# Kernel optimization log

Measured on AMD Instinct MI355X. Metric: run time of the kernel, lower is better.

Reference implementation:

```python
import jax, jax.numpy as jnp
import numpy as np

N = {'QENT': 20000, 'CENT': 50000, 'SPAN': 40000, 'SENT': 40000}
E = 250000
IN_DIM, HID = 256, 128
NEG_SLOPE = 0.2  # GATConv default negative_slope
RELS = [('QENT', 'SPAN'), ('QENT', 'SENT'), ('CENT', 'SENT'), ('SPAN', 'CENT'), ('CENT', 'CENT')]
ENAMES = ['e_qent_span', 'e_qent_sent', 'e_cent_sent', 'e_span_cent', 'e_cent_cooccur']


def setup_inputs() -> dict:
    key = jax.random.key(0)
    ks = jax.random.split(key, 20)
    inp = {}
    for i, t in enumerate(['QENT', 'CENT', 'SPAN', 'SENT']):
        inp['x_' + t] = jax.random.normal(ks[i], (N[t], IN_DIM), jnp.float32)
    for i, (nm, (s, d)) in enumerate(zip(ENAMES, RELS)):
        k1, k2 = jax.random.split(ks[4 + i])
        src = jax.random.randint(k1, (E,), 0, N[s])
        dst = jax.random.randint(k2, (E,), 0, N[d])
        inp[nm] = jnp.stack([src, dst]).astype(jnp.int32)
    inp['lin_W'] = jax.random.normal(ks[10], (4, IN_DIM, HID), jnp.float32) / np.sqrt(IN_DIM).astype(np.float32)
    inp['lin_b'] = jnp.zeros((4, HID), jnp.float32)
    inp['conv_Ws'] = jax.random.normal(ks[11], (2, 5, HID, HID), jnp.float32) / np.sqrt(HID).astype(np.float32)
    inp['conv_Wd'] = jax.random.normal(ks[12], (2, 5, HID, HID), jnp.float32) / np.sqrt(HID).astype(np.float32)
    inp['conv_as'] = jax.random.normal(ks[13], (2, 5, HID), jnp.float32) / np.sqrt(HID).astype(np.float32)
    inp['conv_ad'] = jax.random.normal(ks[14], (2, 5, HID), jnp.float32) / np.sqrt(HID).astype(np.float32)
    inp['conv_b'] = jnp.zeros((2, 5, HID), jnp.float32)
    inp['out_W'] = jax.random.normal(ks[15], (HID, 1), jnp.float32) / np.sqrt(HID).astype(np.float32)
    inp['out_b'] = jnp.zeros((1,), jnp.float32)
    return inp


def _gat(x_src, x_dst, edge, Ws, Wd, a_s, a_d, b, n_dst):
    """PyG GATConv, heads=1, concat=True, add_self_loops=False, bipartite lin_src/lin_dst."""
    hs = x_src @ Ws                       # [Ns, H]
    hd = x_dst @ Wd                       # [Nd, H]
    src, dst = edge[0], edge[1]
    e = jax.nn.leaky_relu((hs @ a_s)[src] + (hd @ a_d)[dst], NEG_SLOPE)  # [E]
    m = jax.ops.segment_max(e, dst, num_segments=n_dst)
    m = jnp.where(jnp.isfinite(m), m, 0.0)
    ex = jnp.exp(e - m[dst])
    denom = jax.ops.segment_sum(ex, dst, num_segments=n_dst)
    alpha = ex / (denom[dst] + 1e-16)     # segment softmax (PyG adds 1e-16)
    out = jax.ops.segment_sum(alpha[:, None] * hs[src], dst, num_segments=n_dst)
    return out + b


def _forward(x_QENT, x_CENT, x_SPAN, x_SENT,
             e_qent_span, e_qent_sent, e_cent_sent, e_span_cent, e_cent_cooccur,
             lin_W, lin_b, conv_Ws, conv_Wd, conv_as, conv_ad, conv_b, out_W, out_b):
    # per-type input projection (pyg Linear has bias)
    x = {'QENT': x_QENT @ lin_W[0] + lin_b[0],
         'CENT': x_CENT @ lin_W[1] + lin_b[1],
         'SPAN': x_SPAN @ lin_W[2] + lin_b[2],
         'SENT': x_SENT @ lin_W[3] + lin_b[3]}
    for l in range(2):
        p = lambda r: (conv_Ws[l, r], conv_Wd[l, r], conv_as[l, r], conv_ad[l, r], conv_b[l, r])
        span = _gat(x['QENT'], x['SPAN'], e_qent_span, *p(0), N['SPAN'])
        sent = (_gat(x['QENT'], x['SENT'], e_qent_sent, *p(1), N['SENT'])
                + _gat(x['CENT'], x['SENT'], e_cent_sent, *p(2), N['SENT']))  # HeteroConv aggr='sum'
        cent = (_gat(x['SPAN'], x['CENT'], e_span_cent, *p(3), N['CENT'])
                + _gat(x['CENT'], x['CENT'], e_cent_cooccur, *p(4), N['CENT']))
        x = {'QENT': x['QENT'],  # QENT has no incoming edges; carried through so layer 2 can use it as source
             'SPAN': jax.nn.relu(span),
             'SENT': jax.nn.relu(sent),
             'CENT': jax.nn.relu(cent)}
    return (x['SPAN'] @ out_W + out_b)[:, 0]  # squeeze(-1) -> [N_SPAN]


def reference(x_QENT, x_CENT, x_SPAN, x_SENT,
              e_qent_span, e_qent_sent, e_cent_sent, e_span_cent, e_cent_cooccur,
              lin_W, lin_b, conv_Ws, conv_Wd, conv_as, conv_ad, conv_b, out_W, out_b):
    return _forward(x_QENT, x_CENT, x_SPAN, x_SENT,
                    e_qent_span, e_qent_sent, e_cent_sent, e_span_cent, e_cent_cooccur,
                    lin_W, lin_b, conv_Ws, conv_Wd, conv_as, conv_ad, conv_b, out_W, out_b)
```

## Files before the change

kernel.cpp:

```cpp
#include <hip/hip_runtime.h>
#include <hip/hip_fp16.h>

#define IN_DIM 256
#define HID 128
#define ELLW 16
#define OVF_CAP 32768

using bf16x8 = __attribute__((ext_vector_type(8))) short;
using f32x4 = __attribute__((ext_vector_type(4))) float;

struct h8 { __half2 a, b, c, d; };

__device__ __forceinline__ unsigned short f2bf(float f) {
    unsigned u = __float_as_uint(f);
    u += 0x7fffu + ((u >> 16) & 1u);
    return (unsigned short)(u >> 16);
}

template <int CTRL>
__device__ __forceinline__ float dpp_rot(float x) {
    return __int_as_float(
        __builtin_amdgcn_update_dpp(0, __float_as_int(x), CTRL, 0xf, 0xf, false));
}
__device__ __forceinline__ float rsum16(float x) {
    x += dpp_rot<0x121>(x);
    x += dpp_rot<0x122>(x);
    x += dpp_rot<0x124>(x);
    x += dpp_rot<0x128>(x);
    return x;
}
__device__ __forceinline__ float rmax16(float x) {
    x = fmaxf(x, dpp_rot<0x121>(x));
    x = fmaxf(x, dpp_rot<0x122>(x));
    x = fmaxf(x, dpp_rot<0x124>(x));
    x = fmaxf(x, dpp_rot<0x128>(x));
    return x;
}

__device__ __forceinline__ void accum8(f32x4& a0, f32x4& a1, float a, const h8& hv) {
    const float2 f0 = __half22float2(hv.a);
    const float2 f1 = __half22float2(hv.b);
    const float2 f2 = __half22float2(hv.c);
    const float2 f3 = __half22float2(hv.d);
    a0[0] += a * f0.x; a0[1] += a * f0.y;
    a0[2] += a * f1.x; a0[3] += a * f1.y;
    a1[0] += a * f2.x; a1[1] += a * f2.y;
    a1[2] += a * f3.x; a1[3] += a * f3.y;
}

__device__ __forceinline__ float epilogue16(const f32x4& a0, const f32x4& a1,
                                            const float* __restrict__ bias,
                                            const float* __restrict__ dvec, int sl) {
    const f32x4 bb0 = *reinterpret_cast<const f32x4*>(bias + sl * 8);
    const f32x4 bb1 = *reinterpret_cast<const f32x4*>(bias + sl * 8 + 4);
    const f32x4 d0 = *reinterpret_cast<const f32x4*>(dvec + sl * 8);
    const f32x4 d1 = *reinterpret_cast<const f32x4*>(dvec + sl * 8 + 4);
    float q = 0.f;
#pragma unroll
    for (int i = 0; i < 4; ++i) {
        q += fmaxf(a0[i] + bb0[i], 0.f) * d0[i];
        q += fmaxf(a1[i] + bb1[i], 0.f) * d1[i];
    }
    return rsum16(q);
}

__device__ __forceinline__ void wt_cvt_one(const float* __restrict__ W,
                                           short* __restrict__ Wt, int idx) {
    const int kkblk = idx >> 10;
    const int n = (idx >> 3) & 127;
    const int t = idx & 7;
    const int k = (kkblk << 3) | t;
    Wt[idx] = (short)f2bf(W[(size_t)k * HID + n]);
}

__global__ __launch_bounds__(256) void setup_k(const float* __restrict__ lin_W,
                                               const float* __restrict__ lin_b,
                                               const float* __restrict__ conv_Ws,
                                               const float* __restrict__ Wd,
                                               const float* __restrict__ adv,
                                               short* __restrict__ wtl,
                                               short* __restrict__ wtc0,
                                               short* __restrict__ wtc5,
                                               float* __restrict__ wd_out,
                                               float* __restrict__ v2,
                                               float* __restrict__ c2,
                                               int* __restrict__ deg,
                                               int* __restrict__ ell,
                                               int* __restrict__ ovf_cnt, int NS, int zd) {
    const int b = blockIdx.x;
    if (b < 256) {
        const int idx = b * 256 + threadIdx.x;
        if (idx < 32768) {
            wt_cvt_one(lin_W, wtl, idx);
        } else if (idx < 49152) {
            wt_cvt_one(conv_Ws, wtc0, idx - 32768);
        } else {
            wt_cvt_one(conv_Ws + 5 * (size_t)HID * HID, wtc5, idx - 49152);
        }
    } else if (b == 256) {
        __shared__ float wd1s[HID];
        const int t = threadIdx.x;
        const int l = t >> 7, j = t & 127;
        const float* w = Wd + ((size_t)(l * 5) * HID + j) * HID;
        const float* a = adv + (size_t)(l * 5) * HID;
        float s = 0.f;
        for (int k = 0; k < HID; k += 4) {
            const float4 wv = *reinterpret_cast<const float4*>(w + k);
            const float4 av = *reinterpret_cast<const float4*>(a + k);
            s += wv.x * av.x + wv.y * av.y + wv.z * av.z + wv.w * av.w;
        }
        wd_out[t] = s;
        if (l == 0) wd1s[j] = s;
        __syncthreads();
        const float* wr = lin_W + 2 * (size_t)IN_DIM * HID + (size_t)t * HID;
        float p = 0.f;
        for (int k = 0; k < HID; k += 4) {
            const float4 wv = *reinterpret_cast<const float4*>(wr + k);
            p += wv.x * wd1s[k] + wv.y * wd1s[k + 1] + wv.z * wd1s[k + 2] +
                 wv.w * wd1s[k + 3];
        }
        v2[t] = p;
        if (t == 0) {
            const float* br = lin_b + 2 * HID;
            float q = 0.f;
            for (int k = 0; k < HID; ++k) q += br[k] * wd1s[k];
            c2[0] = q;
        }
        if (t == 1) ovf_cnt[0] = 0;
    } else if (b < 257 + zd) {
        const int i4 = ((b - 257) * 256 + threadIdx.x) * 4;
        if (i4 + 4 <= NS) {
            *reinterpret_cast<int4*>(deg + i4) = make_int4(0, 0, 0, 0);
        } else {
            for (int i = i4; i < NS; ++i) deg[i] = 0;
        }
    } else {
        const int total = NS * ELLW;
        const int i4 = ((b - 257 - zd) * 256 + threadIdx.x) * 4;
        if (i4 + 4 <= total) *reinterpret_cast<int4*>(ell + i4) = make_int4(0, 0, 0, 0);
    }
}

template <int K>
__device__ __forceinline__ void gemm_body(const float* __restrict__ A,
                                          const short* __restrict__ Wt,
                                          const float* __restrict__ bias,
                                          float* __restrict__ C, int N, int bid) {
    const int tid = threadIdx.x;
    const int w = tid >> 6;
    const int lane = tid & 63;
    const int m16 = lane & 15;
    const int kg = lane >> 4;

    const int arow = bid * 64 + w * 16 + m16;
    const bool ok = arow < N;

    f32x4 acc[8];
#pragma unroll
    for (int j = 0; j < 8; ++j) acc[j] = (f32x4){0.f, 0.f, 0.f, 0.f};

    for (int k0 = 0; k0 < K; k0 += 32) {
        bf16x8 af = {0, 0, 0, 0, 0, 0, 0, 0};
        if (ok) {
            const float* ap = A + (size_t)arow * K + k0 + kg * 8;
            const float4 f0 = *reinterpret_cast<const float4*>(ap);
            const float4 f1 = *reinterpret_cast<const float4*>(ap + 4);
            af[0] = (short)f2bf(f0.x); af[1] = (short)f2bf(f0.y);
            af[2] = (short)f2bf(f0.z); af[3] = (short)f2bf(f0.w);
            af[4] = (short)f2bf(f1.x); af[5] = (short)f2bf(f1.y);
            af[6] = (short)f2bf(f1.z); af[7] = (short)f2bf(f1.w);
        }
        const short* bbase = Wt + (((k0 >> 3) + kg) << 10);
#pragma unroll
        for (int j = 0; j < 8; ++j) {
            const bf16x8 bf = *reinterpret_cast<const bf16x8*>(bbase + ((j * 16 + m16) << 3));
            acc[j] = __builtin_amdgcn_mfma_f32_16x16x32_bf16(af, bf, acc[j], 0, 0, 0);
        }
    }

    const int rbase = bid * 64 + w * 16 + kg * 4;
    float bj[8];
#pragma unroll
    for (int j = 0; j < 8; ++j) bj[j] = bias ? bias[j * 16 + m16] : 0.f;
#pragma unroll
    for (int j = 0; j < 8; ++j)
#pragma unroll
        for (int r = 0; r < 4; ++r) {
            const int row = rbase + r;
            if (row < N) C[(size_t)row * HID + j * 16 + m16] = acc[j][r] + bj[j];
        }
}

__global__ __launch_bounds__(256) void build_gemm_k(const int* __restrict__ src,
                                                    const int* __restrict__ dst, int E,
                                                    int* __restrict__ deg,
                                                    int* __restrict__ ell,
                                                    int2* __restrict__ ovf,
                                                    int* __restrict__ ovf_cnt,
                                                    const float* __restrict__ A,
                                                    const short* __restrict__ Wt,
                                                    const float* __restrict__ bias,
                                                    float* __restrict__ C, int N, int eb) {
    if ((int)blockIdx.x < eb) {
        const int e = blockIdx.x * 256 + threadIdx.x;
        if (e < E) {
            const int d = dst[e], s = src[e];
            const int pos = atomicAdd(deg + d, 1);
            if (pos < ELLW) {
                ell[(size_t)d * ELLW + pos] = s;
            } else {
                const int oi = atomicAdd(ovf_cnt, 1);
                if (oi < OVF_CAP) ovf[oi] = make_int2(d, s);
            }
        }
    } else {
        gemm_body<IN_DIM>(A, Wt, bias, C, N, (int)blockIdx.x - eb);
    }
}

__global__ __launch_bounds__(256) void gemm_dual_k(const float* __restrict__ A,
                                                   const short* __restrict__ Wt0,
                                                   const short* __restrict__ Wt1,
                                                   __half* __restrict__ C,
                                                   float* __restrict__ as1,
                                                   float* __restrict__ as2,
                                                   const float* __restrict__ a1v,
                                                   const float* __restrict__ a2v, int N) {
    const int tid = threadIdx.x;
    const int w = tid >> 6;
    const int lane = tid & 63;
    const int m16 = lane & 15;
    const int kg = lane >> 4;

    const int arow = blockIdx.x * 64 + w * 16 + m16;
    const bool ok = arow < N;

    f32x4 acc[16];
#pragma unroll
    for (int j = 0; j < 16; ++j) acc[j] = (f32x4){0.f, 0.f, 0.f, 0.f};

    for (int k0 = 0; k0 < HID; k0 += 32) {
        bf16x8 af = {0, 0, 0, 0, 0, 0, 0, 0};
        if (ok) {
            const float* ap = A + (size_t)arow * HID + k0 + kg * 8;
            const float4 f0 = *reinterpret_cast<const float4*>(ap);
            const float4 f1 = *reinterpret_cast<const float4*>(ap + 4);
            af[0] = (short)f2bf(f0.x); af[1] = (short)f2bf(f0.y);
            af[2] = (short)f2bf(f0.z); af[3] = (short)f2bf(f0.w);
            af[4] = (short)f2bf(f1.x); af[5] = (short)f2bf(f1.y);
            af[6] = (short)f2bf(f1.z); af[7] = (short)f2bf(f1.w);
        }
        const int boff = ((k0 >> 3) + kg) << 10;
        const short* b0 = Wt0 + boff;
        const short* b1 = Wt1 + boff;
#pragma unroll
        for (int j = 0; j < 8; ++j) {
            const bf16x8 bf0 = *reinterpret_cast<const bf16x8*>(b0 + ((j * 16 + m16) << 3));
            acc[j] = __builtin_amdgcn_mfma_f32_16x16x32_bf16(af, bf0, acc[j], 0, 0, 0);
            const bf16x8 bf1 = *reinterpret_cast<const bf16x8*>(b1 + ((j * 16 + m16) << 3));
            acc[j + 8] = __builtin_amdgcn_mfma_f32_16x16x32_bf16(af, bf1, acc[j + 8], 0, 0, 0);
        }
    }

    const int rbase = blockIdx.x * 64 + w * 16 + kg * 4;
#pragma unroll
    for (int j = 0; j < 16; ++j)
#pragma unroll
        for (int r = 0; r < 4; ++r) {
            const int row = rbase + r;
            if (row < N) C[(size_t)row * 256 + j * 16 + m16] = __float2half(acc[j][r]);
        }

    float p1[4] = {0.f, 0.f, 0.f, 0.f};
    float p2[4] = {0.f, 0.f, 0.f, 0.f};
#pragma unroll
    for (int j = 0; j < 8; ++j) {
        const float a1 = a1v[j * 16 + m16];
        const float a2 = a2v[j * 16 + m16];
#pragma unroll
        for (int r = 0; r < 4; ++r) {
            p1[r] += acc[j][r] * a1;
            p2[r] += acc[j + 8][r] * a2;
        }
    }
#pragma unroll
    for (int r = 0; r < 4; ++r) {
        p1[r] = rsum16(p1[r]);
        p2[r] = rsum16(p2[r]);
    }
    if (m16 == 0)
#pragma unroll
        for (int r = 0; r < 4; ++r) {
            const int row = rbase + r;
            if (row < N) {
                as1[row] = p1[r];
                as2[row] = p2[r];
            }
        }
}

__global__ __launch_bounds__(256, 4) void gat_fused_k(
    const int* __restrict__ deg_arr, const int* __restrict__ ell,
    const int2* __restrict__ ovf, const int* __restrict__ ovf_cnt_p,
    const float* __restrict__ x_span, const float* __restrict__ v2,
    const float* __restrict__ c2, const float* __restrict__ as1,
    const float* __restrict__ as2, const __half* __restrict__ hs,
    const float* __restrict__ b1, const float* __restrict__ wd2v,
    const float* __restrict__ b2, const float* __restrict__ outW,
    const float* __restrict__ outb, float* __restrict__ out, int Ndst) {
    const int gidx = blockIdx.x * blockDim.x + threadIdx.x;
    const int row = gidx >> 4;
    const int sl = threadIdx.x & 15;
    const int grp = threadIdx.x & 48;
    if (row >= Ndst) return;

    const int deg = deg_arr[row];
    const int ce = ell[(size_t)row * ELLW + sl];

    float p = 0.f;
    const float* xr = x_span + (size_t)row * IN_DIM + sl * 16;
    const float* vr = v2 + sl * 16;
#pragma unroll
    for (int i = 0; i < 4; ++i) {
        const float4 xv = *reinterpret_cast<const float4*>(xr + i * 4);
        const float4 vv = *reinterpret_cast<const float4*>(vr + i * 4);
        p += xv.x * vv.x + xv.y * vv.y + xv.z * vv.z + xv.w * vv.w;
    }
    const float ad1 = rsum16(p) + c2[0];

    const float a1c = as1[ce];
    const float a2c = as2[ce];

    h8 h1[8], h2[8];
#pragma unroll
    for (int i = 0; i < 8; ++i) {
        const int s = __shfl(ce, grp | i, 64);
        const __half* hb = hs + (size_t)s * 256 + sl * 8;
        h1[i] = *reinterpret_cast<const h8*>(hb);
        h2[i] = *reinterpret_cast<const h8*>(hb + 128);
    }

    if (deg <= ELLW) {
        float t1 = a1c + ad1;
        t1 = t1 > 0.f ? t1 : 0.2f * t1;
        const float ex1 = (sl < deg) ? __expf(t1) : 0.f;
        const float al1 = ex1 / (rsum16(ex1) + 1e-16f);

        f32x4 acc0 = {0.f, 0.f, 0.f, 0.f}, acc1 = {0.f, 0.f, 0.f, 0.f};
#pragma unroll
        for (int i = 0; i < 8; ++i) {
            const float a = __shfl(al1, grp | i, 64);
            accum8(acc0, acc1, a, h1[i]);
        }
        for (int i = 8; i < deg; ++i) {
            const int s = __shfl(ce, grp | i, 64);
            const float a = __shfl(al1, grp | i, 64);
            const h8 hv = *reinterpret_cast<const h8*>(hs + (size_t)s * 256 + sl * 8);
            accum8(acc0, acc1, a, hv);
        }
        const float ad2 = epilogue16(acc0, acc1, b1, wd2v, sl);

        float t2 = a2c + ad2;
        t2 = t2 > 0.f ? t2 : 0.2f * t2;
        const float ex2 = (sl < deg) ? __expf(t2) : 0.f;
        const float al2 = ex2 / (rsum16(ex2) + 1e-16f);

        f32x4 bcc0 = {0.f, 0.f, 0.f, 0.f}, bcc1 = {0.f, 0.f, 0.f, 0.f};
#pragma unroll
        for (int i = 0; i < 8; ++i) {
            const float a = __shfl(al2, grp | i, 64);
            accum8(bcc0, bcc1, a, h2[i]);
        }
        for (int i = 8; i < deg; ++i) {
            const int s = __shfl(ce, grp | i, 64);
            const float a = __shfl(al2, grp | i, 64);
            const h8 hv = *reinterpret_cast<const h8*>(hs + (size_t)s * 256 + 128 + sl * 8);
            accum8(bcc0, bcc1, a, hv);
        }
        const float q = epilogue16(bcc0, bcc1, b2, outW, sl);
        if (sl == 0) out[row] = q + outb[0];
    } else {
        int oc = *ovf_cnt_p;
        if (oc > OVF_CAP) oc = OVF_CAP;
        float ad = ad1;
#pragma unroll
        for (int layer = 0; layer < 2; ++layer) {
            const float ac = layer ? a2c : a1c;
            const float* as_s = layer ? as2 : as1;
            const int hoff = layer ? HID : 0;
            const float* bias = layer ? b2 : b1;
            const float* dvec = layer ? outW : wd2v;

            float te = ac + ad;
            te = te > 0.f ? te : 0.2f * te;
            float m = rmax16(te);
            for (int i = 0; i < oc; ++i) {
                const int2 o = ovf[i];
                if (o.x == row) {
                    float t = as_s[o.y] + ad;
                    t = t > 0.f ? t : 0.2f * t;
                    m = fmaxf(m, t);
                }
            }
            const float ex = __expf(te - m);
            float dsum = rsum16(ex);
            for (int i = 0; i < oc; ++i) {
                const int2 o = ovf[i];
                if (o.x == row) {
                    float t = as_s[o.y] + ad;
                    t = t > 0.f ? t : 0.2f * t;
                    dsum += __expf(t - m);
                }
            }
            const float inv = 1.f / (dsum + 1e-16f);
            const float al = ex * inv;

            f32x4 acc0 = {0.f, 0.f, 0.f, 0.f}, acc1 = {0.f, 0.f, 0.f, 0.f};
#pragma unroll
            for (int i = 0; i < 16; ++i) {
                const int s = __shfl(ce, grp | i, 64);
                const float a = __shfl(al, grp | i, 64);
                const h8 hv =
                    *reinterpret_cast<const h8*>(hs + (size_t)s * 256 + hoff + sl * 8);
                accum8(acc0, acc1, a, hv);
            }
            for (int i = 0; i < oc; ++i) {
                const int2 o = ovf[i];
                if (o.x == row) {
                    float t = as_s[o.y] + ad;
                    t = t > 0.f ? t : 0.2f * t;
                    const float a = __expf(t - m) * inv;
                    const h8 hv =
                        *reinterpret_cast<const h8*>(hs + (size_t)o.y * 256 + hoff + sl * 8);
                    accum8(acc0, acc1, a, hv);
                }
            }
            const float q = epilogue16(acc0, acc1, bias, dvec, sl);
            if (layer == 0) {
                ad = q;
            } else if (sl == 0) {
                out[row] = q + outb[0];
            }
        }
    }
}

extern "C" void kernel_launch(void* const* d_in, const int* in_sizes, int n_in,
                              void* d_out, int out_size, void* d_ws, size_t ws_size,
                              hipStream_t stream) {
    const float* x_qent = (const float*)d_in[0];
    const float* x_span = (const float*)d_in[2];
    const int* e_qs = (const int*)d_in[4];
    const float* lin_W = (const float*)d_in[9];
    const float* lin_b = (const float*)d_in[10];
    const float* conv_Ws = (const float*)d_in[11];
    const float* conv_Wd = (const float*)d_in[12];
    const float* conv_as = (const float*)d_in[13];
    const float* conv_ad = (const float*)d_in[14];
    const float* conv_b = (const float*)d_in[15];
    const float* out_W = (const float*)d_in[16];
    const float* out_b = (const float*)d_in[17];

    const int NQ = in_sizes[0] / IN_DIM;
    const int NS = in_sizes[2] / IN_DIM;
    const int E = in_sizes[4] / 2;
    const int* srcp = e_qs;
    const int* dstp = e_qs + E;
    (void)n_in; (void)out_size;

    float* ws = (float*)d_ws;
    size_t off = 0;
    auto alloc = [&](size_t n) {
        n = (n + 3) & ~(size_t)3;
        float* p = ws + off;
        off += n;
        return p;
    };
    float* xq = alloc((size_t)NQ * HID);
    __half* hs = (__half*)alloc((size_t)NQ * 128);
    float* as1 = alloc(NQ);
    float* as2 = alloc(NQ);
    float* wd2 = alloc(2 * HID);
    float* v2 = alloc(IN_DIM);
    float* c2 = alloc(1);
    int* deg = (int*)alloc(NS);
    int* ell = (int*)alloc((size_t)NS * ELLW);
    int2* ovf = (int2*)alloc(2 * OVF_CAP);
    int* ovf_cnt = (int*)alloc(1);
    short* wt_lin0 = (short*)alloc(IN_DIM * HID / 2);
    short* wt_conv0 = (short*)alloc(HID * HID / 2);
    short* wt_conv5 = (short*)alloc(HID * HID / 2);
    (void)ws_size;

    const int zd = (NS + 1023) / 1024;
    const int ze = (NS * ELLW + 1023) / 1024;
    setup_k<<<dim3(257 + zd + ze), dim3(256), 0, stream>>>(
        lin_W, lin_b, conv_Ws, conv_Wd, conv_ad, wt_lin0, wt_conv0, wt_conv5, wd2, v2, c2,
        deg, ell, ovf_cnt, NS, zd);

    const int eb = (E + 255) / 256;
    const int gb = (NQ + 63) / 64;
    build_gemm_k<<<dim3(eb + gb), dim3(256), 0, stream>>>(
        srcp, dstp, E, deg, ell, ovf, ovf_cnt, x_qent, wt_lin0, lin_b, xq, NQ, eb);

    gemm_dual_k<<<dim3(gb), dim3(256), 0, stream>>>(
        xq, wt_conv0, wt_conv5, hs, as1, as2, conv_as, conv_as + 5 * (size_t)HID, NQ);

    gat_fused_k<<<dim3(((size_t)NS * 16 + 255) / 256), dim3(256), 0, stream>>>(
        deg, ell, ovf, ovf_cnt, x_span, v2, c2, as1, as2, hs, conv_b, wd2 + HID,
        conv_b + 5 * (size_t)HID, out_W, out_b, (float*)d_out, NS);
}
```

Before: 96.04 us.

## Prefetch all 16 ELL neighbors per row with vector loads and explicit scheduling

In the common deg<=16 path, each lane now loads the whole 16-entry ELL row as int4 vectors and issues all 16 layer-1 neighbor feature loads and attention scalar loads up front. It then computes the softmax per lane in registers, dropping the cross-lane shuffles and the serial tail loop for neighbors beyond 8. Layer-2 feature loads are issued before the layer-1 accumulation, and sched_barriers keep these loads grouped so their memory latency overlaps. In exchange the register footprint grows sharply and launch bounds drop from 4 to 2 blocks per SM, which lowers occupancy and may spill.

```diff
diff --git a/kernel.cpp b/kernel.cpp
--- a/kernel.cpp
+++ b/kernel.cpp
@@ -36,6 +36,8 @@
     x = fmaxf(x, dpp_rot<0x128>(x));
     return x;
 }
+
+__device__ __forceinline__ float lrelu(float t) { return t > 0.f ? t : 0.2f * t; }
 
 __device__ __forceinline__ void accum8(f32x4& a0, f32x4& a1, float a, const h8& hv) {
     const float2 f0 = __half22float2(hv.a);
@@ -299,7 +301,12 @@
         }
 }
 
-__global__ __launch_bounds__(256, 4) void gat_fused_k(
+#define ELIST(OP) OP(0, e0.x) OP(1, e0.y) OP(2, e0.z) OP(3, e0.w) \
+                  OP(4, e1.x) OP(5, e1.y) OP(6, e1.z) OP(7, e1.w) \
+                  OP(8, e2.x) OP(9, e2.y) OP(10, e2.z) OP(11, e2.w) \
+                  OP(12, e3.x) OP(13, e3.y) OP(14, e3.z) OP(15, e3.w)
+
+__global__ __launch_bounds__(256, 2) void gat_fused_k(
     const int* __restrict__ deg_arr, const int* __restrict__ ell,
     const int2* __restrict__ ovf, const int* __restrict__ ovf_cnt_p,
     const float* __restrict__ x_span, const float* __restrict__ v2,
@@ -311,78 +318,94 @@
     const int gidx = blockIdx.x * blockDim.x + threadIdx.x;
     const int row = gidx >> 4;
     const int sl = threadIdx.x & 15;
-    const int grp = threadIdx.x & 48;
     if (row >= Ndst) return;
 
     const int deg = deg_arr[row];
-    const int ce = ell[(size_t)row * ELLW + sl];
-
-    float p = 0.f;
-    const float* xr = x_span + (size_t)row * IN_DIM + sl * 16;
-    const float* vr = v2 + sl * 16;
-#pragma unroll
-    for (int i = 0; i < 4; ++i) {
-        const float4 xv = *reinterpret_cast<const float4*>(xr + i * 4);
-        const float4 vv = *reinterpret_cast<const float4*>(vr + i * 4);
-        p += xv.x * vv.x + xv.y * vv.y + xv.z * vv.z + xv.w * vv.w;
-    }
-    const float ad1 = rsum16(p) + c2[0];
-
-    const float a1c = as1[ce];
-    const float a2c = as2[ce];
-
-    h8 h1[8], h2[8];
-#pragma unroll
-    for (int i = 0; i < 8; ++i) {
-        const int s = __shfl(ce, grp | i, 64);
-        const __half* hb = hs + (size_t)s * 256 + sl * 8;
-        h1[i] = *reinterpret_cast<const h8*>(hb);
-        h2[i] = *reinterpret_cast<const h8*>(hb + 128);
-    }
 
     if (deg <= ELLW) {
-        float t1 = a1c + ad1;
-        t1 = t1 > 0.f ? t1 : 0.2f * t1;
-        const float ex1 = (sl < deg) ? __expf(t1) : 0.f;
-        const float al1 = ex1 / (rsum16(ex1) + 1e-16f);
+        const int* erow = ell + (size_t)row * ELLW;
+        const int4 e0 = *reinterpret_cast<const int4*>(erow);
+        const int4 e1 = *reinterpret_cast<const int4*>(erow + 4);
+        const int4 e2 = *reinterpret_cast<const int4*>(erow + 8);
+        const int4 e3 = *reinterpret_cast<const int4*>(erow + 12);
+
+        const float* xr = x_span + (size_t)row * IN_DIM + sl * 16;
+        const float* vr = v2 + sl * 16;
+        float4 xv[4], vv[4];
+#pragma unroll
+        for (int i = 0; i < 4; ++i) {
+            xv[i] = *reinterpret_cast<const float4*>(xr + i * 4);
+            vv[i] = *reinterpret_cast<const float4*>(vr + i * 4);
+        }
+
+#define DECL_AS(i, s) const float as1v_##i = as1[s]; const float as2v_##i = as2[s];
+        ELIST(DECL_AS)
+#undef DECL_AS
+#define DECL_H1(i, s) \
+        const h8 h1_##i = *reinterpret_cast<const h8*>(hs + (size_t)(s) * 256 + sl * 8);
+        ELIST(DECL_H1)
+#undef DECL_H1
+        __builtin_amdgcn_sched_barrier(0);
+
+        float p = 0.f;
+#pragma unroll
+        for (int i = 0; i < 4; ++i)
+            p += xv[i].x * vv[i].x + xv[i].y * vv[i].y + xv[i].z * vv[i].z +
+                 xv[i].w * vv[i].w;
+        const float ad1 = rsum16(p) + c2[0];
+
+        float dsum1 = 0.f;
+#define AL1(i, s) \
+        float al1_##i = (i < deg) ? __expf(lrelu(as1v_##i + ad1)) : 0.f; dsum1 += al1_##i;
+        ELIST(AL1)
+#undef AL1
+        const float inv1 = 1.f / (dsum1 + 1e-16f);
+
+#define DECL_H2(i, s) \
+        const h8 h2_##i = \
+            *reinterpret_cast<const h8*>(hs + (size_t)(s) * 256 + 128 + sl * 8);
+        ELIST(DECL_H2)
+#undef DECL_H2
+        __builtin_amdgcn_sched_barrier(0);
 
         f32x4 acc0 = {0.f, 0.f, 0.f, 0.f}, acc1 = {0.f, 0.f, 0.f, 0.f};
-#pragma unroll
-        for (int i = 0; i < 8; ++i) {
-            const float a = __shfl(al1, grp | i, 64);
-            accum8(acc0, acc1, a, h1[i]);
-        }
-        for (int i = 8; i < deg; ++i) {
-            const int s = __shfl(ce, grp | i, 64);
-            const float a = __shfl(al1, grp | i, 64);
-            const h8 hv = *reinterpret_cast<const h8*>(hs + (size_t)s * 256 + sl * 8);
-            accum8(acc0, acc1, a, hv);
-        }
+#define ACC1(i, s) accum8(acc0, acc1, al1_##i * inv1, h1_##i);
+        ELIST(ACC1)
+#undef ACC1
         const float ad2 = epilogue16(acc0, acc1, b1, wd2v, sl);
 
-        float t2 = a2c + ad2;
-        t2 = t2 > 0.f ? t2 : 0.2f * t2;
-        const float ex2 = (sl < deg) ? __expf(t2) : 0.f;
-        const float al2 = ex2 / (rsum16(ex2) + 1e-16f);
+        float dsum2 = 0.f;
+#define AL2(i, s) \
+        float al2_##i = (i < deg) ? __expf(lrelu(as2v_##i + ad2)) : 0.f; dsum2 += al2_##i;
+        ELIST(AL2)
+#undef AL2
+        const float inv2 = 1.f / (dsum2 + 1e-16f);
 
         f32x4 bcc0 = {0.f, 0.f, 0.f, 0.f}, bcc1 = {0.f, 0.f, 0.f, 0.f};
-#pragma unroll
-        for (int i = 0; i < 8; ++i) {
-            const float a = __shfl(al2, grp | i, 64);
-            accum8(bcc0, bcc1, a, h2[i]);
-        }
-        for (int i = 8; i < deg; ++i) {
-            const int s = __shfl(ce, grp | i, 64);
-            const float a = __shfl(al2, grp | i, 64);
-            const h8 hv = *reinterpret_cast<const h8*>(hs + (size_t)s * 256 + 128 + sl * 8);
-            accum8(bcc0, bcc1, a, hv);
-        }
+#define ACC2(i, s) accum8(bcc0, bcc1, al2_##i * inv2, h2_##i);
+        ELIST(ACC2)
+#undef ACC2
         const float q = epilogue16(bcc0, bcc1, b2, outW, sl);
         if (sl == 0) out[row] = q + outb[0];
     } else {
+        const int grp = threadIdx.x & 48;
+        const int ce = ell[(size_t)row * ELLW + sl];
+        const float a1c = as1[ce];
+        const float a2c = as2[ce];
+
+        float p = 0.f;
+        const float* xr = x_span + (size_t)row * IN_DIM + sl * 16;
+        const float* vr = v2 + sl * 16;
+#pragma unroll
+        for (int i = 0; i < 4; ++i) {
+            const float4 xv = *reinterpret_cast<const float4*>(xr + i * 4);
+            const float4 vv = *reinterpret_cast<const float4*>(vr + i * 4);
+            p += xv.x * vv.x + xv.y * vv.y + xv.z * vv.z + xv.w * vv.w;
+        }
+        float ad = rsum16(p) + c2[0];
+
         int oc = *ovf_cnt_p;
         if (oc > OVF_CAP) oc = OVF_CAP;
-        float ad = ad1;
 #pragma unroll
         for (int layer = 0; layer < 2; ++layer) {
             const float ac = layer ? a2c : a1c;
@@ -391,26 +414,17 @@
             const float* bias = layer ? b2 : b1;
             const float* dvec = layer ? outW : wd2v;
 
-            float te = ac + ad;
-            te = te > 0.f ? te : 0.2f * te;
+            float te = lrelu(ac + ad);
             float m = rmax16(te);
             for (int i = 0; i < oc; ++i) {
                 const int2 o = ovf[i];
-                if (o.x == row) {
-                    float t = as_s[o.y] + ad;
-                    t = t > 0.f ? t : 0.2f * t;
-                    m = fmaxf(m, t);
-                }
+                if (o.x == row) m = fmaxf(m, lrelu(as_s[o.y] + ad));
             }
             const float ex = __expf(te - m);
             float dsum = rsum16(ex);
             for (int i = 0; i < oc; ++i) {
                 const int2 o = ovf[i];
-                if (o.x == row) {
-                    float t = as_s[o.y] + ad;
-                    t = t > 0.f ? t : 0.2f * t;
-                    dsum += __expf(t - m);
-                }
+                if (o.x == row) dsum += __expf(lrelu(as_s[o.y] + ad) - m);
             }
             const float inv = 1.f / (dsum + 1e-16f);
             const float al = ex * inv;
@@ -427,9 +441,7 @@
             for (int i = 0; i < oc; ++i) {
                 const int2 o = ovf[i];
                 if (o.x == row) {
-                    float t = as_s[o.y] + ad;
-                    t = t > 0.f ? t : 0.2f * t;
-                    const float a = __expf(t - m) * inv;
+                    const float a = __expf(lrelu(as_s[o.y] + ad) - m) * inv;
                     const h8 hv =
                         *reinterpret_cast<const h8*>(hs + (size_t)o.y * 256 + hoff + sl * 8);
                     accum8(acc0, acc1, a, hv);
```

Measured after the change: 101.4 us. 1.06x slower.

## Fold QENT linear into conv weights and fuse two GEMMs into one

Applied to the files above, without the earlier changes.

Precomputes the combined weight lin_W·conv_Ws (and the combined bias) for both layers in the setup kernel, so the QENT projection and the two conv source projections become a single K=256 GEMM running inside the edge-build kernel. This removes the gemm_dual_k launch and the fp32 xq intermediate round trip. It also interleaves the per-layer hs halves per lane and packs the two attention scalars into one float2 to make gathers more local. The trade-offs are a larger GEMM (K=256 with 256 output columns), a slower setup kernel that computes 65k dot products of length 128, and different rounding from bf16-quantizing the product weights.

```diff
diff --git a/kernel.cpp b/kernel.cpp
--- a/kernel.cpp
+++ b/kernel.cpp
@@ -36,6 +36,8 @@
     x = fmaxf(x, dpp_rot<0x128>(x));
     return x;
 }
+
+__device__ __forceinline__ float lrelu(float t) { return t > 0.f ? t : 0.2f * t; }
 
 __device__ __forceinline__ void accum8(f32x4& a0, f32x4& a1, float a, const h8& hv) {
     const float2 f0 = __half22float2(hv.a);
@@ -64,23 +66,14 @@
     return rsum16(q);
 }
 
-__device__ __forceinline__ void wt_cvt_one(const float* __restrict__ W,
-                                           short* __restrict__ Wt, int idx) {
-    const int kkblk = idx >> 10;
-    const int n = (idx >> 3) & 127;
-    const int t = idx & 7;
-    const int k = (kkblk << 3) | t;
-    Wt[idx] = (short)f2bf(W[(size_t)k * HID + n]);
-}
-
 __global__ __launch_bounds__(256) void setup_k(const float* __restrict__ lin_W,
                                                const float* __restrict__ lin_b,
                                                const float* __restrict__ conv_Ws,
                                                const float* __restrict__ Wd,
                                                const float* __restrict__ adv,
-                                               short* __restrict__ wtl,
-                                               short* __restrict__ wtc0,
-                                               short* __restrict__ wtc5,
+                                               short* __restrict__ wt0,
+                                               short* __restrict__ wt1,
+                                               float* __restrict__ bc,
                                                float* __restrict__ wd_out,
                                                float* __restrict__ v2,
                                                float* __restrict__ c2,
@@ -90,14 +83,28 @@
     const int b = blockIdx.x;
     if (b < 256) {
         const int idx = b * 256 + threadIdx.x;
-        if (idx < 32768) {
-            wt_cvt_one(lin_W, wtl, idx);
-        } else if (idx < 49152) {
-            wt_cvt_one(conv_Ws, wtc0, idx - 32768);
-        } else {
-            wt_cvt_one(conv_Ws + 5 * (size_t)HID * HID, wtc5, idx - 49152);
-        }
+        const int l = idx >> 15;
+        const int rem = idx & 32767;
+        const int k = rem >> 7;
+        const int n = rem & 127;
+        const float* lw = lin_W + (size_t)k * HID;
+        const float* cw = conv_Ws + (size_t)(l * 5) * HID * HID + n;
+        float s = 0.f;
+#pragma unroll 4
+        for (int m = 0; m < HID; ++m) s += lw[m] * cw[(size_t)m * HID];
+        short* wt = l ? wt1 : wt0;
+        wt[((k >> 3) << 10) + (n << 3) + (k & 7)] = (short)f2bf(s);
     } else if (b == 256) {
+        const int t = threadIdx.x;
+        const int l = t >> 7;
+        const int n = t & 127;
+        const float* cw = conv_Ws + (size_t)(l * 5) * HID * HID + n;
+        float s = 0.f;
+#pragma unroll 4
+        for (int m = 0; m < HID; ++m) s += lin_b[m] * cw[(size_t)m * HID];
+        bc[t] = s;
+        if (t == 0) ovf_cnt[0] = 0;
+    } else if (b == 257) {
         __shared__ float wd1s[HID];
         const int t = threadIdx.x;
         const int l = t >> 7, j = t & 127;
@@ -126,9 +133,8 @@
             for (int k = 0; k < HID; ++k) q += br[k] * wd1s[k];
             c2[0] = q;
         }
-        if (t == 1) ovf_cnt[0] = 0;
-    } else if (b < 257 + zd) {
-        const int i4 = ((b - 257) * 256 + threadIdx.x) * 4;
+    } else if (b < 258 + zd) {
+        const int i4 = ((b - 258) * 256 + threadIdx.x) * 4;
         if (i4 + 4 <= NS) {
             *reinterpret_cast<int4*>(deg + i4) = make_int4(0, 0, 0, 0);
         } else {
@@ -136,71 +142,19 @@
         }
     } else {
         const int total = NS * ELLW;
-        const int i4 = ((b - 257 - zd) * 256 + threadIdx.x) * 4;
+        const int i4 = ((b - 258 - zd) * 256 + threadIdx.x) * 4;
         if (i4 + 4 <= total) *reinterpret_cast<int4*>(ell + i4) = make_int4(0, 0, 0, 0);
     }
 }
 
-template <int K>
-__device__ __forceinline__ void gemm_body(const float* __restrict__ A,
-                                          const short* __restrict__ Wt,
-                                          const float* __restrict__ bias,
-                                          float* __restrict__ C, int N, int bid) {
-    const int tid = threadIdx.x;
-    const int w = tid >> 6;
-    const int lane = tid & 63;
-    const int m16 = lane & 15;
-    const int kg = lane >> 4;
-
-    const int arow = bid * 64 + w * 16 + m16;
-    const bool ok = arow < N;
-
-    f32x4 acc[8];
-#pragma unroll
-    for (int j = 0; j < 8; ++j) acc[j] = (f32x4){0.f, 0.f, 0.f, 0.f};
-
-    for (int k0 = 0; k0 < K; k0 += 32) {
-        bf16x8 af = {0, 0, 0, 0, 0, 0, 0, 0};
-        if (ok) {
-            const float* ap = A + (size_t)arow * K + k0 + kg * 8;
-            const float4 f0 = *reinterpret_cast<const float4*>(ap);
-            const float4 f1 = *reinterpret_cast<const float4*>(ap + 4);
-            af[0] = (short)f2bf(f0.x); af[1] = (short)f2bf(f0.y);
-            af[2] = (short)f2bf(f0.z); af[3] = (short)f2bf(f0.w);
-            af[4] = (short)f2bf(f1.x); af[5] = (short)f2bf(f1.y);
-            af[6] = (short)f2bf(f1.z); af[7] = (short)f2bf(f1.w);
-        }
-        const short* bbase = Wt + (((k0 >> 3) + kg) << 10);
-#pragma unroll
-        for (int j = 0; j < 8; ++j) {
-            const bf16x8 bf = *reinterpret_cast<const bf16x8*>(bbase + ((j * 16 + m16) << 3));
-            acc[j] = __builtin_amdgcn_mfma_f32_16x16x32_bf16(af, bf, acc[j], 0, 0, 0);
-        }
-    }
-
-    const int rbase = bid * 64 + w * 16 + kg * 4;
-    float bj[8];
-#pragma unroll
-    for (int j = 0; j < 8; ++j) bj[j] = bias ? bias[j * 16 + m16] : 0.f;
-#pragma unroll
-    for (int j = 0; j < 8; ++j)
-#pragma unroll
-        for (int r = 0; r < 4; ++r) {
-            const int row = rbase + r;
-            if (row < N) C[(size_t)row * HID + j * 16 + m16] = acc[j][r] + bj[j];
-        }
-}
-
-__global__ __launch_bounds__(256) void build_gemm_k(const int* __restrict__ src,
-                                                    const int* __restrict__ dst, int E,
-                                                    int* __restrict__ deg,
-                                                    int* __restrict__ ell,
-                                                    int2* __restrict__ ovf,
-                                                    int* __restrict__ ovf_cnt,
-                                                    const float* __restrict__ A,
-                                                    const short* __restrict__ Wt,
-                                                    const float* __restrict__ bias,
-                                                    float* __restrict__ C, int N, int eb) {
+__global__ __launch_bounds__(256) void build_gemm_k(
+    const int* __restrict__ src, const int* __restrict__ dst, int E,
+    int* __restrict__ deg, int* __restrict__ ell, int2* __restrict__ ovf,
+    int* __restrict__ ovf_cnt, const float* __restrict__ A,
+    const short* __restrict__ Wt0, const short* __restrict__ Wt1,
+    const float* __restrict__ bc, __half* __restrict__ hs,
+    float2* __restrict__ as12, const float* __restrict__ a1v,
+    const float* __restrict__ a2v, int N, int eb) {
     if ((int)blockIdx.x < eb) {
         const int e = blockIdx.x * 256 + threadIdx.x;
         if (e < E) {
@@ -213,36 +167,26 @@
                 if (oi < OVF_CAP) ovf[oi] = make_int2(d, s);
             }
         }
-    } else {
-        gemm_body<IN_DIM>(A, Wt, bias, C, N, (int)blockIdx.x - eb);
-    }
-}
-
-__global__ __launch_bounds__(256) void gemm_dual_k(const float* __restrict__ A,
-                                                   const short* __restrict__ Wt0,
-                                                   const short* __restrict__ Wt1,
-                                                   __half* __restrict__ C,
-                                                   float* __restrict__ as1,
-                                                   float* __restrict__ as2,
-                                                   const float* __restrict__ a1v,
-                                                   const float* __restrict__ a2v, int N) {
+        return;
+    }
+    const int bid = (int)blockIdx.x - eb;
     const int tid = threadIdx.x;
     const int w = tid >> 6;
     const int lane = tid & 63;
     const int m16 = lane & 15;
     const int kg = lane >> 4;
 
-    const int arow = blockIdx.x * 64 + w * 16 + m16;
+    const int arow = bid * 64 + w * 16 + m16;
     const bool ok = arow < N;
 
     f32x4 acc[16];
 #pragma unroll
     for (int j = 0; j < 16; ++j) acc[j] = (f32x4){0.f, 0.f, 0.f, 0.f};
 
-    for (int k0 = 0; k0 < HID; k0 += 32) {
+    for (int k0 = 0; k0 < IN_DIM; k0 += 32) {
         bf16x8 af = {0, 0, 0, 0, 0, 0, 0, 0};
         if (ok) {
-            const float* ap = A + (size_t)arow * HID + k0 + kg * 8;
+            const float* ap = A + (size_t)arow * IN_DIM + k0 + kg * 8;
             const float4 f0 = *reinterpret_cast<const float4*>(ap);
             const float4 f1 = *reinterpret_cast<const float4*>(ap + 4);
             af[0] = (short)f2bf(f0.x); af[1] = (short)f2bf(f0.y);
@@ -262,25 +206,28 @@
         }
     }
 
-    const int rbase = blockIdx.x * 64 + w * 16 + kg * 4;
-#pragma unroll
-    for (int j = 0; j < 16; ++j)
+    const int rbase = bid * 64 + w * 16 + kg * 4;
+    float p1[4] = {0.f, 0.f, 0.f, 0.f};
+    float p2[4] = {0.f, 0.f, 0.f, 0.f};
+#pragma unroll
+    for (int j = 0; j < 8; ++j) {
+        const int col = j * 16 + m16;
+        const float b0v = bc[col];
+        const float b1v = bc[128 + col];
+        const float a1 = a1v[col];
+        const float a2 = a2v[col];
+        const int so = j * 32 + ((m16 >> 3) << 4) + (m16 & 7);
 #pragma unroll
         for (int r = 0; r < 4; ++r) {
             const int row = rbase + r;
-            if (row < N) C[(size_t)row * 256 + j * 16 + m16] = __float2half(acc[j][r]);
-        }
-
-    float p1[4] = {0.f, 0.f, 0.f, 0.f};
-    float p2[4] = {0.f, 0.f, 0.f, 0.f};
-#pragma unroll
-    for (int j = 0; j < 8; ++j) {
-        const float a1 = a1v[j * 16 + m16];
-        const float a2 = a2v[j * 16 + m16];
-#pragma unroll
-        for (int r = 0; r < 4; ++r) {
-            p1[r] += acc[j][r] * a1;
-            p2[r] += acc[j + 8][r] * a2;
+            const float v1 = acc[j][r] + b0v;
+            const float v2v = acc[j + 8][r] + b1v;
+            if (row < N) {
+                hs[(size_t)row * 256 + so] = __float2half(v1);
+                hs[(size_t)row * 256 + so + 8] = __float2half(v2v);
+            }
+            p1[r] += v1 * a1;
+            p2[r] += v2v * a2;
         }
     }
 #pragma unroll
@@ -292,10 +239,7 @@
 #pragma unroll
         for (int r = 0; r < 4; ++r) {
             const int row = rbase + r;
-            if (row < N) {
-                as1[row] = p1[r];
-                as2[row] = p2[r];
-            }
+            if (row < N) as12[row] = make_float2(p1[r], p2[r]);
         }
 }
 
@@ -303,11 +247,11 @@
     const int* __restrict__ deg_arr, const int* __restrict__ ell,
     const int2* __restrict__ ovf, const int* __restrict__ ovf_cnt_p,
     const float* __restrict__ x_span, const float* __restrict__ v2,
-    const float* __restrict__ c2, const float* __restrict__ as1,
-    const float* __restrict__ as2, const __half* __restrict__ hs,
-    const float* __restrict__ b1, const float* __restrict__ wd2v,
-    const float* __restrict__ b2, const float* __restrict__ outW,
-    const float* __restrict__ outb, float* __restrict__ out, int Ndst) {
+    const float* __restrict__ c2, const float2* __restrict__ as12,
+    const __half* __restrict__ hs, const float* __restrict__ b1,
+    const float* __restrict__ wd2v, const float* __restrict__ b2,
+    const float* __restrict__ outW, const float* __restrict__ outb,
+    float* __restrict__ out, int Ndst) {
     const int gidx = blockIdx.x * blockDim.x + threadIdx.x;
     const int row = gidx >> 4;
     const int sl = threadIdx.x & 15;
@@ -328,22 +272,21 @@
     }
     const float ad1 = rsum16(p) + c2[0];
 
-    const float a1c = as1[ce];
-    const float a2c = as2[ce];
+    const float2 asv = as12[ce];
+    const float a1c = asv.x;
+    const float a2c = asv.y;
 
     h8 h1[8], h2[8];
 #pragma unroll
     for (int i = 0; i < 8; ++i) {
         const int s = __shfl(ce, grp | i, 64);
-        const __half* hb = hs + (size_t)s * 256 + sl * 8;
+        const __half* hb = hs + (size_t)s * 256 + sl * 16;
         h1[i] = *reinterpret_cast<const h8*>(hb);
-        h2[i] = *reinterpret_cast<const h8*>(hb + 128);
+        h2[i] = *reinterpret_cast<const h8*>(hb + 8);
     }
 
     if (deg <= ELLW) {
-        float t1 = a1c + ad1;
-        t1 = t1 > 0.f ? t1 : 0.2f * t1;
-        const float ex1 = (sl < deg) ? __expf(t1) : 0.f;
+        const float ex1 = (sl < deg) ? __expf(lrelu(a1c + ad1)) : 0.f;
         const float al1 = ex1 / (rsum16(ex1) + 1e-16f);
 
         f32x4 acc0 = {0.f, 0.f, 0.f, 0.f}, acc1 = {0.f, 0.f, 0.f, 0.f};
@@ -355,14 +298,12 @@
         for (int i = 8; i < deg; ++i) {
             const int s = __shfl(ce, grp | i, 64);
             const float a = __shfl(al1, grp | i, 64);
-            const h8 hv = *reinterpret_cast<const h8*>(hs + (size_t)s * 256 + sl * 8);
+            const h8 hv = *reinterpret_cast<const h8*>(hs + (size_t)s * 256 + sl * 16);
             accum8(acc0, acc1, a, hv);
         }
         const float ad2 = epilogue16(acc0, acc1, b1, wd2v, sl);
 
-        float t2 = a2c + ad2;
-        t2 = t2 > 0.f ? t2 : 0.2f * t2;
-        const float ex2 = (sl < deg) ? __expf(t2) : 0.f;
+        const float ex2 = (sl < deg) ? __expf(lrelu(a2c + ad2)) : 0.f;
         const float al2 = ex2 / (rsum16(ex2) + 1e-16f);
 
         f32x4 bcc0 = {0.f, 0.f, 0.f, 0.f}, bcc1 = {0.f, 0.f, 0.f, 0.f};
@@ -374,7 +315,7 @@
         for (int i = 8; i < deg; ++i) {
             const int s = __shfl(ce, grp | i, 64);
             const float a = __shfl(al2, grp | i, 64);
-            const h8 hv = *reinterpret_cast<const h8*>(hs + (size_t)s * 256 + 128 + sl * 8);
+            const h8 hv = *reinterpret_cast<const h8*>(hs + (size_t)s * 256 + sl * 16 + 8);
             accum8(bcc0, bcc1, a, hv);
         }
         const float q = epilogue16(bcc0, bcc1, b2, outW, sl);
@@ -386,20 +327,17 @@
 #pragma unroll
         for (int layer = 0; layer < 2; ++layer) {
             const float ac = layer ? a2c : a1c;
-            const float* as_s = layer ? as2 : as1;
-            const int hoff = layer ? HID : 0;
+            const int ho = layer ? 8 : 0;
             const float* bias = layer ? b2 : b1;
             const float* dvec = layer ? outW : wd2v;
 
-            float te = ac + ad;
-            te = te > 0.f ? te : 0.2f * te;
+            float te = lrelu(ac + ad);
             float m = rmax16(te);
             for (int i = 0; i < oc; ++i) {
                 const int2 o = ovf[i];
                 if (o.x == row) {
-                    float t = as_s[o.y] + ad;
-                    t = t > 0.f ? t : 0.2f * t;
-                    m = fmaxf(m, t);
+                    const float2 oas = as12[o.y];
+                    m = fmaxf(m, lrelu((layer ? oas.y : oas.x) + ad));
                 }
             }
             const float ex = __expf(te - m);
@@ -407,9 +345,8 @@
             for (int i = 0; i < oc; ++i) {
                 const int2 o = ovf[i];
                 if (o.x == row) {
-                    float t = as_s[o.y] + ad;
-                    t = t > 0.f ? t : 0.2f * t;
-                    dsum += __expf(t - m);
+                    const float2 oas = as12[o.y];
+                    dsum += __expf(lrelu((layer ? oas.y : oas.x) + ad) - m);
                 }
             }
             const float inv = 1.f / (dsum + 1e-16f);
@@ -421,17 +358,16 @@
                 const int s = __shfl(ce, grp | i, 64);
                 const float a = __shfl(al, grp | i, 64);
                 const h8 hv =
-                    *reinterpret_cast<const h8*>(hs + (size_t)s * 256 + hoff + sl * 8);
+                    *reinterpret_cast<const h8*>(hs + (size_t)s * 256 + sl * 16 + ho);
                 accum8(acc0, acc1, a, hv);
             }
             for (int i = 0; i < oc; ++i) {
                 const int2 o = ovf[i];
                 if (o.x == row) {
-                    float t = as_s[o.y] + ad;
-                    t = t > 0.f ? t : 0.2f * t;
-                    const float a = __expf(t - m) * inv;
+                    const float2 oas = as12[o.y];
+                    const float a = __expf(lrelu((layer ? oas.y : oas.x) + ad) - m) * inv;
                     const h8 hv =
-                        *reinterpret_cast<const h8*>(hs + (size_t)o.y * 256 + hoff + sl * 8);
+                        *reinterpret_cast<const h8*>(hs + (size_t)o.y * 256 + sl * 16 + ho);
                     accum8(acc0, acc1, a, hv);
                 }
             }
@@ -476,37 +412,33 @@
         off += n;
         return p;
     };
-    float* xq = alloc((size_t)NQ * HID);
     __half* hs = (__half*)alloc((size_t)NQ * 128);
-    float* as1 = alloc(NQ);
-    float* as2 = alloc(NQ);
+    float2* as12 = (float2*)alloc(2 * (size_t)NQ);
     float* wd2 = alloc(2 * HID);
     float* v2 = alloc(IN_DIM);
     float* c2 = alloc(1);
+    float* bc = alloc(2 * HID);
     int* deg = (int*)alloc(NS);
     int* ell = (int*)alloc((size_t)NS * ELLW);
     int2* ovf = (int2*)alloc(2 * OVF_CAP);
     int* ovf_cnt = (int*)alloc(1);
-    short* wt_lin0 = (short*)alloc(IN_DIM * HID / 2);
-    short* wt_conv0 = (short*)alloc(HID * HID / 2);
-    short* wt_conv5 = (short*)alloc(HID * HID / 2);
+    short* wt0 = (short*)alloc(IN_DIM * HID / 2);
+    short* wt1 = (short*)alloc(IN_DIM * HID / 2);
     (void)ws_size;
 
     const int zd = (NS + 1023) / 1024;
     const int ze = (NS * ELLW + 1023) / 1024;
-    setup_k<<<dim3(257 + zd + ze), dim3(256), 0, stream>>>(
-        lin_W, lin_b, conv_Ws, conv_Wd, conv_ad, wt_lin0, wt_conv0, wt_conv5, wd2, v2, c2,
-        deg, ell, ovf_cnt, NS, zd);
+    setup_k<<<dim3(258 + zd + ze), dim3(256), 0, stream>>>(
+        lin_W, lin_b, conv_Ws, conv_Wd, conv_ad, wt0, wt1, bc, wd2, v2, c2, deg, ell,
+        ovf_cnt, NS, zd);
 
     const int eb = (E + 255) / 256;
     const int gb = (NQ + 63) / 64;
     build_gemm_k<<<dim3(eb + gb), dim3(256), 0, stream>>>(
-        srcp, dstp, E, deg, ell, ovf, ovf_cnt, x_qent, wt_lin0, lin_b, xq, NQ, eb);
-
-    gemm_dual_k<<<dim3(gb), dim3(256), 0, stream>>>(
-        xq, wt_conv0, wt_conv5, hs, as1, as2, conv_as, conv_as + 5 * (size_t)HID, NQ);
+        srcp, dstp, E, deg, ell, ovf, ovf_cnt, x_qent, wt0, wt1, bc, hs, as12, conv_as,
+        conv_as + 5 * (size_t)HID, NQ, eb);
 
     gat_fused_k<<<dim3(((size_t)NS * 16 + 255) / 256), dim3(256), 0, stream>>>(
-        deg, ell, ovf, ovf_cnt, x_span, v2, c2, as1, as2, hs, conv_b, wd2 + HID,
+        deg, ell, ovf, ovf_cnt, x_span, v2, c2, as12, hs, conv_b, wd2 + HID,
         conv_b + 5 * (size_t)HID, out_W, out_b, (float*)d_out, NS);
 }
```

After: 86.63 us. 1.11x faster.
